# Performance work log

Hardware: AMD Instinct MI355X
Metric: run time of the kernel (lower is better)

## Reference

```python
import jax, jax.numpy as jnp
import numpy as np

D_MODEL = 1024
NHEAD = 16
HEAD_DIM = D_MODEL // NHEAD
WINDOW = 33  # mask keeps |i-j| > WINDOW//2 (True = attend, matching torch SDPA bool-mask semantics)


def setup_inputs() -> dict:
    key = jax.random.key(0)
    ks = jax.random.split(key, 9)
    s = 1.0 / np.sqrt(D_MODEL)
    x = jax.random.normal(ks[0], (2, 2048, D_MODEL), dtype=jnp.float32)
    Wq = jax.random.uniform(ks[1], (D_MODEL, D_MODEL), jnp.float32, -s, s)
    bq = jax.random.uniform(ks[2], (D_MODEL,), jnp.float32, -s, s)
    Wk = jax.random.uniform(ks[3], (D_MODEL, D_MODEL), jnp.float32, -s, s)
    bk = jax.random.uniform(ks[4], (D_MODEL,), jnp.float32, -s, s)
    Wv = jax.random.uniform(ks[5], (D_MODEL, D_MODEL), jnp.float32, -s, s)
    bv = jax.random.uniform(ks[6], (D_MODEL,), jnp.float32, -s, s)
    Wo = jax.random.uniform(ks[7], (D_MODEL, D_MODEL), jnp.float32, -s, s)
    bo = jax.random.uniform(ks[8], (D_MODEL,), jnp.float32, -s, s)
    return {"x": x, "Wq": Wq, "bq": bq, "Wk": Wk, "bk": bk,
            "Wv": Wv, "bv": bv, "Wo": Wo, "bo": bo}


def reference(x, Wq, bq, Wk, bk, Wv, bv, Wo, bo):
    B, T, C = x.shape
    H, D = NHEAD, HEAD_DIM
    # projections (torch Linear: y = x @ W.T + b)
    q = (x @ Wq.T + bq).reshape(B, T, H, D).transpose(0, 2, 1, 3)  # [B,H,T,D]
    k = (x @ Wk.T + bk).reshape(B, T, H, D).transpose(0, 2, 1, 3)
    v = (x @ Wv.T + bv).reshape(B, T, H, D).transpose(0, 2, 1, 3)
    idx = jnp.arange(T)
    rel = jnp.abs(idx[:, None] - idx[None, :])
    keep = rel > (WINDOW // 2)  # True = participate (torch SDPA bool-mask semantics)
    scale = 1.0 / jnp.sqrt(jnp.asarray(D, dtype=x.dtype))
    scores = jnp.einsum('bhqd,bhkd->bhqk', q, k) * scale
    scores = jnp.where(keep, scores, jnp.asarray(-jnp.inf, dtype=scores.dtype))
    attn = jax.nn.softmax(scores, axis=-1)
    out = jnp.einsum('bhqk,bhkd->bhqd', attn, v)  # [B,H,T,D]
    out = out.transpose(0, 2, 1, 3).reshape(B, T, C)
    return out @ Wo.T + bo
```

## Files before the change

kernel.cpp:

```cpp
#include <hip/hip_runtime.h>
#include <stdint.h>


typedef unsigned short u16;
typedef short bf16x8 __attribute__((ext_vector_type(8)));
typedef float f32x4 __attribute__((ext_vector_type(4)));

#define MFMA16 __builtin_amdgcn_mfma_f32_16x16x32_bf16

__device__ __forceinline__ u16 f2bf(float f) {
  union { float f; uint32_t u; } v; v.f = f;
  return (u16)((v.u + 0x7fffu + ((v.u >> 16) & 1u)) >> 16);
}

__device__ __forceinline__ uint32_t cvt_pk_bf16(float lo, float hi) {
  uint32_t d;
  asm("v_cvt_pk_bf16_f32 %0, %1, %2" : "=v"(d) : "v"(lo), "v"(hi));
  return d;
}

__global__ void f2b_kernel(const float* __restrict__ in, u16* __restrict__ out, int n4) {
  int i = blockIdx.x * blockDim.x + threadIdx.x;
  if (i < n4) {
    float4 v = reinterpret_cast<const float4*>(in)[i];
    ushort4 o;
    o.x = f2bf(v.x); o.y = f2bf(v.y); o.z = f2bf(v.z); o.w = f2bf(v.w);
    reinterpret_cast<ushort4*>(out)[i] = o;
  }
}

__global__ void f2b4_kernel(const float* __restrict__ a, const float* __restrict__ b,
                            const float* __restrict__ c, const float* __restrict__ d,
                            u16* __restrict__ oa, u16* __restrict__ ob,
                            u16* __restrict__ oc, u16* __restrict__ od, int n4) {
  int i = blockIdx.x * blockDim.x + threadIdx.x;
  if (i >= n4) return;
  int w = blockIdx.y;
  const float* src = (w == 0) ? a : (w == 1) ? b : (w == 2) ? c : d;
  u16* dst = (w == 0) ? oa : (w == 1) ? ob : (w == 2) ? oc : od;
  float4 v = reinterpret_cast<const float4*>(src)[i];
  ushort4 o;
  o.x = f2bf(v.x); o.y = f2bf(v.y); o.z = f2bf(v.z); o.w = f2bf(v.w);
  reinterpret_cast<ushort4*>(dst)[i] = o;
}

#define GEMM_LOAD(REGA, REGB, A_, B_, KOFF)                                                        \
  do {                                                                                             \
    REGA##0 = *reinterpret_cast<const uint4*>(A_ + (size_t)(gm_base +  0) * 1024 + (KOFF) + sslot * 8); \
    REGA##1 = *reinterpret_cast<const uint4*>(A_ + (size_t)(gm_base + 32) * 1024 + (KOFF) + sslot * 8); \
    REGA##2 = *reinterpret_cast<const uint4*>(A_ + (size_t)(gm_base + 64) * 1024 + (KOFF) + sslot * 8); \
    REGA##3 = *reinterpret_cast<const uint4*>(A_ + (size_t)(gm_base + 96) * 1024 + (KOFF) + sslot * 8); \
    REGB##0 = *reinterpret_cast<const uint4*>(B_ + (size_t)(gn_base +  0) * 1024 + (KOFF) + sslot * 8); \
    REGB##1 = *reinterpret_cast<const uint4*>(B_ + (size_t)(gn_base + 32) * 1024 + (KOFF) + sslot * 8); \
    REGB##2 = *reinterpret_cast<const uint4*>(B_ + (size_t)(gn_base + 64) * 1024 + (KOFF) + sslot * 8); \
    REGB##3 = *reinterpret_cast<const uint4*>(B_ + (size_t)(gn_base + 96) * 1024 + (KOFF) + sslot * 8); \
  } while (0)

#define GEMM_PUBLISH()                                                                             \
  do {                                                                                             \
    *reinterpret_cast<uint4*>((char*)As + (srow +  0) * 144 + sslot * 16) = ar0;                   \
    *reinterpret_cast<uint4*>((char*)As + (srow + 32) * 144 + sslot * 16) = ar1;                   \
    *reinterpret_cast<uint4*>((char*)As + (srow + 64) * 144 + sslot * 16) = ar2;                   \
    *reinterpret_cast<uint4*>((char*)As + (srow + 96) * 144 + sslot * 16) = ar3;                   \
    *reinterpret_cast<uint4*>((char*)Bs + (srow +  0) * 144 + sslot * 16) = br0;                   \
    *reinterpret_cast<uint4*>((char*)Bs + (srow + 32) * 144 + sslot * 16) = br1;                   \
    *reinterpret_cast<uint4*>((char*)Bs + (srow + 64) * 144 + sslot * 16) = br2;                   \
    *reinterpret_cast<uint4*>((char*)Bs + (srow + 96) * 144 + sslot * 16) = br3;                   \
  } while (0)

#define GEMM_CORE(A_, B_, bm0_, bn0_)                                                              \
  constexpr int KP = 72;                                                                           \
  __shared__ __align__(16) u16 As[128 * KP];                                                       \
  __shared__ __align__(16) u16 Bs[128 * KP];                                                       \
  const int t = threadIdx.x;                                                                       \
  const int lane = t & 63;                                                                         \
  const int wv = t >> 6;                                                                           \
  const int wm = (wv >> 1) * 64;                                                                   \
  const int wn = (wv & 1) * 64;                                                                    \
  const int lg = lane >> 4;                                                                        \
  const int lr = lane & 15;                                                                        \
  const int srow = t >> 3;                                                                         \
  const int sslot = t & 7;                                                                         \
  const int gm_base = bm0_ + srow;                                                                 \
  const int gn_base = bn0_ + srow;                                                                 \
  uint4 ar0, ar1, ar2, ar3, br0, br1, br2, br3;                                                    \
  f32x4 acc[4][4];                                                                                 \
  for (int i = 0; i < 4; ++i)                                                                      \
    for (int j = 0; j < 4; ++j) acc[i][j] = (f32x4)0.0f;                                           \
  GEMM_LOAD(ar, br, A_, B_, 0);                                                                    \
  for (int k0 = 0; k0 < 1024; k0 += 64) {                                                          \
    GEMM_PUBLISH();                                                                                \
    __syncthreads();                                                                               \
    if (k0 + 64 < 1024) GEMM_LOAD(ar, br, A_, B_, k0 + 64);                                        \
    for (int kk = 0; kk < 2; ++kk) {                                                               \
      bf16x8 af[4], bfr[4];                                                                        \
      for (int i = 0; i < 4; ++i)                                                                  \
        af[i] = *reinterpret_cast<const bf16x8*>(&As[(wm + i * 16 + lr) * KP + kk * 32 + lg * 8]); \
      for (int j = 0; j < 4; ++j)                                                                  \
        bfr[j] = *reinterpret_cast<const bf16x8*>(&Bs[(wn + j * 16 + lr) * KP + kk * 32 + lg * 8]);\
      for (int i = 0; i < 4; ++i)                                                                  \
        for (int j = 0; j < 4; ++j)                                                                \
          acc[i][j] = MFMA16(af[i], bfr[j], acc[i][j], 0, 0, 0);                                   \
    }                                                                                              \
    __syncthreads();                                                                               \
  }

__global__ __launch_bounds__(256) void gemm_qkv(
    const u16* __restrict__ A,
    const u16* __restrict__ Wqb, const u16* __restrict__ Wkb, const u16* __restrict__ Wvb,
    const float* __restrict__ bqp, const float* __restrict__ bkp, const float* __restrict__ bvp,
    u16* __restrict__ qo, u16* __restrict__ ko, u16* __restrict__ vo)
{
  const int bid = blockIdx.x + gridDim.x * blockIdx.y;
  const int sid = (bid & 7) * 96 + (bid >> 3);
  const int bm0 = (sid / 24) * 128;
  const int jy = sid % 24;
  const int sel = jy >> 3;
  const int bn0 = (jy & 7) * 128;

  const u16* Bw = (sel == 0) ? Wqb : (sel == 1) ? Wkb : Wvb;
  const float* bias = (sel == 0) ? bqp : (sel == 1) ? bkp : bvp;
  const float scale = (sel == 0) ? 0.125f * 1.44269504f : 1.0f;

  GEMM_CORE(A, Bw, bm0, bn0)

  for (int j = 0; j < 4; ++j) {
    int gn = bn0 + wn + j * 16 + lr;
    float bv = bias[gn];
    for (int i = 0; i < 4; ++i) {
      for (int r = 0; r < 4; ++r) {
        int gm = bm0 + wm + i * 16 + lg * 4 + r;
        float val = (acc[i][j][r] + bv) * scale;
        int b = gm >> 11, tt = gm & 2047;
        int h = gn >> 6,  d = gn & 63;
        u16 o = f2bf(val);
        if (sel == 0)
          qo[((size_t)(b * 16 + h) * 2048 + tt) * 64 + d] = o;
        else if (sel == 1)
          ko[((size_t)(b * 16 + h) * 2048 + tt) * 64 + d] = o;
        else
          vo[((size_t)(b * 16 + h) * 64 + d) * 2048 + tt] = o;
      }
    }
  }
}

__global__ __launch_bounds__(256) void gemm_out(
    const u16* __restrict__ A, const u16* __restrict__ Bw,
    const float* __restrict__ bias, float* __restrict__ outp)
{
  const int bm0 = blockIdx.x * 128;
  const int bn0 = blockIdx.y * 128;

  GEMM_CORE(A, Bw, bm0, bn0)

  for (int j = 0; j < 4; ++j) {
    int gn = bn0 + wn + j * 16 + lr;
    float bv = bias[gn];
    for (int i = 0; i < 4; ++i)
      for (int r = 0; r < 4; ++r) {
        int gm = bm0 + wm + i * 16 + lg * 4 + r;
        outp[(size_t)gm * 1024 + gn] = acc[i][j][r] + bv;
      }
  }
}

__global__ __launch_bounds__(256, 3) void attn_kernel(
    const u16* __restrict__ qb, const u16* __restrict__ kb,
    const u16* __restrict__ vtb, u16* __restrict__ ab)
{
  constexpr int KP = 72;
  __shared__ __align__(16) u16 Kb[2][64 * KP];
  __shared__ __align__(16) u16 Vb[2][64 * KP];
  __shared__ __align__(16) u16 Pl[4][16 * 64];

  const int bid = blockIdx.x + gridDim.x * blockIdx.y;
  const int sid = (bid & 7) * 128 + (bid >> 3);
  const int bx = sid & 31;
  const int bh = sid >> 5;

  const int t = threadIdx.x;
  const int lane = t & 63;
  const int wv = t >> 6;
  const int lg = lane >> 4, lr = lane & 15;
  const int q0 = bx * 64 + wv * 16;

  const u16* Qp = qb + (size_t)bh * 2048 * 64;
  const u16* Kp = kb + (size_t)bh * 2048 * 64;
  const u16* Vt = vtb + (size_t)bh * 64 * 2048;
  char* Pw = (char*)&Pl[wv][0];
  const int swz = (lr & 7) << 4;

  const int sl = lane & 7;
  const int r0 = wv * 16 + (lane >> 3);
  const int sdst0 = r0 * (KP * 2) + sl * 16;

  uint4 krA, krB, vrA, vrB;

#define ISSUE_LOADS(J0N)                                                                 \
  do {                                                                                   \
    krA = *reinterpret_cast<const uint4*>(Kp + (size_t)((J0N) + r0) * 64 + sl * 8);      \
    krB = *reinterpret_cast<const uint4*>(Kp + (size_t)((J0N) + r0 + 8) * 64 + sl * 8);  \
    vrA = *reinterpret_cast<const uint4*>(Vt + (size_t)r0 * 2048 + (J0N) + sl * 8);      \
    vrB = *reinterpret_cast<const uint4*>(Vt + (size_t)(r0 + 8) * 2048 + (J0N) + sl * 8);\
  } while (0)

#define WRITE_LDS(BUF)                                                                   \
  do {                                                                                   \
    *reinterpret_cast<uint4*>((char*)&Kb[BUF][0] + sdst0)                = krA;          \
    *reinterpret_cast<uint4*>((char*)&Kb[BUF][0] + sdst0 + 8 * KP * 2)   = krB;          \
    *reinterpret_cast<uint4*>((char*)&Vb[BUF][0] + sdst0)                = vrA;          \
    *reinterpret_cast<uint4*>((char*)&Vb[BUF][0] + sdst0 + 8 * KP * 2)   = vrB;          \
  } while (0)

  bf16x8 qf0 = *reinterpret_cast<const bf16x8*>(&Qp[(size_t)(q0 + lr) * 64 + lg * 8]);
  bf16x8 qf1 = *reinterpret_cast<const bf16x8*>(&Qp[(size_t)(q0 + lr) * 64 + 32 + lg * 8]);

  f32x4 o[4];
  for (int d = 0; d < 4; ++d) o[d] = (f32x4)0.0f;
  float m = -1e30f;
  float lsum = 0.0f;

  ISSUE_LOADS(0);
  WRITE_LDS(0);
  __syncthreads();
  int cur = 0;

  for (int tt = 0; tt < 32; ++tt) {
    if (tt < 31) ISSUE_LOADS((tt + 1) * 64);
    const int j0 = tt * 64;

    f32x4 s[4];
    for (int kc = 0; kc < 4; ++kc) {
      bf16x8 kf0 = *reinterpret_cast<const bf16x8*>(&Kb[cur][(kc * 16 + lr) * KP + lg * 8]);
      bf16x8 kf1 = *reinterpret_cast<const bf16x8*>(&Kb[cur][(kc * 16 + lr) * KP + 32 + lg * 8]);
      f32x4 z = (f32x4)0.0f;
      z = MFMA16(kf0, qf0, z, 0, 0, 0);
      z = MFMA16(kf1, qf1, z, 0, 0, 0);
      s[kc] = z;
    }
    if (j0 + 63 >= q0 - 16 && j0 <= q0 + 31) {
      for (int kc = 0; kc < 4; ++kc)
        for (int r = 0; r < 4; ++r) {
          int i = q0 + lr;
          int j = j0 + kc * 16 + lg * 4 + r;
          int dd = i - j; if (dd < 0) dd = -dd;
          if (dd <= 16) s[kc][r] = -1e38f;
        }
    }
    f32x4 t4 = __builtin_elementwise_max(__builtin_elementwise_max(s[0], s[1]),
                                         __builtin_elementwise_max(s[2], s[3]));
    float pm = fmaxf(fmaxf(t4[0], t4[1]), fmaxf(t4[2], t4[3]));
    pm = fmaxf(pm, __shfl_xor(pm, 16));
    pm = fmaxf(pm, __shfl_xor(pm, 32));
    if (__any((int)(pm > m + 11.54f))) {
      float mn = fmaxf(m, pm);
      float a = exp2f(m - mn);
      m = mn;
      lsum *= a;
      for (int d = 0; d < 4; ++d) o[d] *= a;
    }
    for (int kc = 0; kc < 4; ++kc) {
      float p0 = exp2f(s[kc][0] - m);
      float p1 = exp2f(s[kc][1] - m);
      float p2 = exp2f(s[kc][2] - m);
      float p3 = exp2f(s[kc][3] - m);
      lsum += (p0 + p1) + (p2 + p3);
      uint2 pk;
      pk.x = cvt_pk_bf16(p0, p1);
      pk.y = cvt_pk_bf16(p2, p3);
      *reinterpret_cast<uint2*>(Pw + ((lr * 128 + kc * 32 + lg * 8) ^ swz)) = pk;
    }
    asm volatile("s_waitcnt lgkmcnt(0)" ::: "memory");
    for (int kh = 0; kh < 2; ++kh) {
      bf16x8 pa = *reinterpret_cast<const bf16x8*>(
          Pw + ((lr * 128 + kh * 64 + lg * 16) ^ swz));
      for (int d = 0; d < 4; ++d) {
        bf16x8 vf = *reinterpret_cast<const bf16x8*>(
            &Vb[cur][(d * 16 + lr) * KP + kh * 32 + lg * 8]);
        o[d] = MFMA16(vf, pa, o[d], 0, 0, 0);
      }
    }
    if (tt < 31) WRITE_LDS(cur ^ 1);
    __syncthreads();
    cur ^= 1;
  }

  lsum += __shfl_xor(lsum, 16);
  lsum += __shfl_xor(lsum, 32);
  float inv = 1.0f / lsum;
  int b = bh >> 4, h = bh & 15;
  size_t rowoff = ((size_t)b * 2048 + q0 + lr) * 1024 + h * 64;
  for (int d = 0; d < 4; ++d) {
    uint2 pk;
    pk.x = cvt_pk_bf16(o[d][0] * inv, o[d][1] * inv);
    pk.y = cvt_pk_bf16(o[d][2] * inv, o[d][3] * inv);
    *reinterpret_cast<uint2*>(&ab[rowoff + d * 16 + lg * 4]) = pk;
  }
#undef ISSUE_LOADS
#undef WRITE_LDS
}

extern "C" void kernel_launch(void* const* d_in, const int* in_sizes, int n_in,
                              void* d_out, int out_size, void* d_ws, size_t ws_size,
                              hipStream_t stream) {
  const float* x  = (const float*)d_in[0];
  const float* Wq = (const float*)d_in[1];
  const float* bq = (const float*)d_in[2];
  const float* Wk = (const float*)d_in[3];
  const float* bk = (const float*)d_in[4];
  const float* Wv = (const float*)d_in[5];
  const float* bv = (const float*)d_in[6];
  const float* Wo = (const float*)d_in[7];
  const float* bo = (const float*)d_in[8];

  u16* ws  = (u16*)d_ws;
  u16* xb  = ws;
  u16* wqb = ws + 4194304;
  u16* wkb = ws + 5242880;
  u16* wvb = ws + 6291456;
  u16* wob = ws + 7340032;
  u16* qbf = ws + 8388608;
  u16* kbf = ws + 12582912;
  u16* vbf = ws + 16777216;
  u16* ab  = xb;

  f2b_kernel<<<4096, 256, 0, stream>>>(x, xb, 1048576);
  f2b4_kernel<<<dim3(1024, 4), 256, 0, stream>>>(Wq, Wk, Wv, Wo, wqb, wkb, wvb, wob, 262144);

  gemm_qkv<<<dim3(32, 24), 256, 0, stream>>>(xb, wqb, wkb, wvb, bq, bk, bv, qbf, kbf, vbf);

  attn_kernel<<<dim3(32, 32), 256, 0, stream>>>(qbf, kbf, vbf, ab);

  gemm_out<<<dim3(32, 8), 256, 0, stream>>>(ab, wob, bo, (float*)d_out);
}
```

Before: 161.3 us.

## Switch attention to 32x32 MFMA tiles with 128-query blocks

The attention kernel now uses 32x32x16 bf16 MFMA. Each wave handles 32 query rows instead of 16 and each block handles 128 queries, so the grid is halved. This doubles the reuse of every K/V tile loaded into LDS and cuts per-tile LDS traffic and global reloads. It also replaces exp2f with the raw v_exp_f32 instruction and drops the occupancy hint from launch bounds, at the cost of more registers per wave and fewer blocks to spread across CUs.

```diff
diff --git a/kernel.cpp b/kernel.cpp
--- a/kernel.cpp
+++ b/kernel.cpp
@@ -5,8 +5,10 @@
 typedef unsigned short u16;
 typedef short bf16x8 __attribute__((ext_vector_type(8)));
 typedef float f32x4 __attribute__((ext_vector_type(4)));
+typedef float f32x16 __attribute__((ext_vector_type(16)));
 
 #define MFMA16 __builtin_amdgcn_mfma_f32_16x16x32_bf16
+#define MFMA32 __builtin_amdgcn_mfma_f32_32x32x16_bf16
 
 __device__ __forceinline__ u16 f2bf(float f) {
   union { float f; uint32_t u; } v; v.f = f;
@@ -17,6 +19,12 @@
   uint32_t d;
   asm("v_cvt_pk_bf16_f32 %0, %1, %2" : "=v"(d) : "v"(lo), "v"(hi));
   return d;
+}
+
+__device__ __forceinline__ float hexp2(float x) {
+  float r;
+  asm("v_exp_f32 %0, %1" : "=v"(r) : "v"(x));
+  return r;
 }
 
 __global__ void f2b_kernel(const float* __restrict__ in, u16* __restrict__ out, int n4) {
@@ -165,31 +173,31 @@
   }
 }
 
-__global__ __launch_bounds__(256, 3) void attn_kernel(
+__global__ __launch_bounds__(256) void attn_kernel(
     const u16* __restrict__ qb, const u16* __restrict__ kb,
     const u16* __restrict__ vtb, u16* __restrict__ ab)
 {
   constexpr int KP = 72;
   __shared__ __align__(16) u16 Kb[2][64 * KP];
   __shared__ __align__(16) u16 Vb[2][64 * KP];
-  __shared__ __align__(16) u16 Pl[4][16 * 64];
+  __shared__ __align__(16) u16 Pl[4][32 * KP];
 
   const int bid = blockIdx.x + gridDim.x * blockIdx.y;
-  const int sid = (bid & 7) * 128 + (bid >> 3);
-  const int bx = sid & 31;
-  const int bh = sid >> 5;
+  const int sid = (bid & 7) * 64 + (bid >> 3);
+  const int bx = sid & 15;
+  const int bh = sid >> 4;
 
   const int t = threadIdx.x;
   const int lane = t & 63;
   const int wv = t >> 6;
-  const int lg = lane >> 4, lr = lane & 15;
-  const int q0 = bx * 64 + wv * 16;
+  const int ql = lane & 31;
+  const int hi = lane >> 5;
+  const int q0 = bx * 128 + wv * 32;
 
   const u16* Qp = qb + (size_t)bh * 2048 * 64;
   const u16* Kp = kb + (size_t)bh * 2048 * 64;
   const u16* Vt = vtb + (size_t)bh * 64 * 2048;
   char* Pw = (char*)&Pl[wv][0];
-  const int swz = (lr & 7) << 4;
 
   const int sl = lane & 7;
   const int r0 = wv * 16 + (lane >> 3);
@@ -213,11 +221,12 @@
     *reinterpret_cast<uint4*>((char*)&Vb[BUF][0] + sdst0 + 8 * KP * 2)   = vrB;          \
   } while (0)
 
-  bf16x8 qf0 = *reinterpret_cast<const bf16x8*>(&Qp[(size_t)(q0 + lr) * 64 + lg * 8]);
-  bf16x8 qf1 = *reinterpret_cast<const bf16x8*>(&Qp[(size_t)(q0 + lr) * 64 + 32 + lg * 8]);
-
-  f32x4 o[4];
-  for (int d = 0; d < 4; ++d) o[d] = (f32x4)0.0f;
+  bf16x8 qf0 = *reinterpret_cast<const bf16x8*>(&Qp[(size_t)(q0 + ql) * 64 +  0 + hi * 8]);
+  bf16x8 qf1 = *reinterpret_cast<const bf16x8*>(&Qp[(size_t)(q0 + ql) * 64 + 16 + hi * 8]);
+  bf16x8 qf2 = *reinterpret_cast<const bf16x8*>(&Qp[(size_t)(q0 + ql) * 64 + 32 + hi * 8]);
+  bf16x8 qf3 = *reinterpret_cast<const bf16x8*>(&Qp[(size_t)(q0 + ql) * 64 + 48 + hi * 8]);
+
+  f32x16 o0 = (f32x16)0.0f, o1 = (f32x16)0.0f;
   float m = -1e30f;
   float lsum = 0.0f;
 
@@ -230,72 +239,87 @@
     if (tt < 31) ISSUE_LOADS((tt + 1) * 64);
     const int j0 = tt * 64;
 
-    f32x4 s[4];
-    for (int kc = 0; kc < 4; ++kc) {
-      bf16x8 kf0 = *reinterpret_cast<const bf16x8*>(&Kb[cur][(kc * 16 + lr) * KP + lg * 8]);
-      bf16x8 kf1 = *reinterpret_cast<const bf16x8*>(&Kb[cur][(kc * 16 + lr) * KP + 32 + lg * 8]);
-      f32x4 z = (f32x4)0.0f;
-      z = MFMA16(kf0, qf0, z, 0, 0, 0);
-      z = MFMA16(kf1, qf1, z, 0, 0, 0);
-      s[kc] = z;
-    }
-    if (j0 + 63 >= q0 - 16 && j0 <= q0 + 31) {
-      for (int kc = 0; kc < 4; ++kc)
-        for (int r = 0; r < 4; ++r) {
-          int i = q0 + lr;
-          int j = j0 + kc * 16 + lg * 4 + r;
-          int dd = i - j; if (dd < 0) dd = -dd;
-          if (dd <= 16) s[kc][r] = -1e38f;
-        }
-    }
-    f32x4 t4 = __builtin_elementwise_max(__builtin_elementwise_max(s[0], s[1]),
-                                         __builtin_elementwise_max(s[2], s[3]));
-    float pm = fmaxf(fmaxf(t4[0], t4[1]), fmaxf(t4[2], t4[3]));
-    pm = fmaxf(pm, __shfl_xor(pm, 16));
+    f32x16 s0 = (f32x16)0.0f, s1 = (f32x16)0.0f;
+    {
+      bf16x8 kf;
+#define QK_STEP(KB, KC, QF, SACC)                                                        \
+      kf = *reinterpret_cast<const bf16x8*>(&Kb[cur][((KB) * 32 + ql) * KP + (KC) * 16 + hi * 8]); \
+      SACC = MFMA32(kf, QF, SACC, 0, 0, 0);
+      QK_STEP(0, 0, qf0, s0) QK_STEP(0, 1, qf1, s0) QK_STEP(0, 2, qf2, s0) QK_STEP(0, 3, qf3, s0)
+      QK_STEP(1, 0, qf0, s1) QK_STEP(1, 1, qf1, s1) QK_STEP(1, 2, qf2, s1) QK_STEP(1, 3, qf3, s1)
+#undef QK_STEP
+    }
+    if (j0 + 63 >= q0 - 16 && j0 <= q0 + 47) {
+      const int i = q0 + ql;
+#pragma unroll
+      for (int reg = 0; reg < 16; ++reg) {
+        int kl = (reg & 3) + 8 * (reg >> 2) + 4 * hi;
+        int d0 = i - (j0 + kl);      if (d0 < 0) d0 = -d0;
+        int d1 = i - (j0 + 32 + kl); if (d1 < 0) d1 = -d1;
+        if (d0 <= 16) s0[reg] = -1e38f;
+        if (d1 <= 16) s1[reg] = -1e38f;
+      }
+    }
+    f32x16 tm = __builtin_elementwise_max(s0, s1);
+    float pm = fmaxf(fmaxf(fmaxf(fmaxf(tm[0], tm[1]), fmaxf(tm[2], tm[3])),
+                           fmaxf(fmaxf(tm[4], tm[5]), fmaxf(tm[6], tm[7]))),
+                     fmaxf(fmaxf(fmaxf(tm[8], tm[9]), fmaxf(tm[10], tm[11])),
+                           fmaxf(fmaxf(tm[12], tm[13]), fmaxf(tm[14], tm[15]))));
     pm = fmaxf(pm, __shfl_xor(pm, 32));
     if (__any((int)(pm > m + 11.54f))) {
       float mn = fmaxf(m, pm);
-      float a = exp2f(m - mn);
+      float a = hexp2(m - mn);
       m = mn;
       lsum *= a;
-      for (int d = 0; d < 4; ++d) o[d] *= a;
-    }
-    for (int kc = 0; kc < 4; ++kc) {
-      float p0 = exp2f(s[kc][0] - m);
-      float p1 = exp2f(s[kc][1] - m);
-      float p2 = exp2f(s[kc][2] - m);
-      float p3 = exp2f(s[kc][3] - m);
-      lsum += (p0 + p1) + (p2 + p3);
-      uint2 pk;
-      pk.x = cvt_pk_bf16(p0, p1);
-      pk.y = cvt_pk_bf16(p2, p3);
-      *reinterpret_cast<uint2*>(Pw + ((lr * 128 + kc * 32 + lg * 8) ^ swz)) = pk;
+      o0 *= a;
+      o1 *= a;
+    }
+    {
+      float psum = 0.0f;
+      char* prow = Pw + ql * (KP * 2);
+#pragma unroll
+      for (int qd = 0; qd < 4; ++qd) {
+        float a0 = hexp2(s0[4 * qd + 0] - m), a1 = hexp2(s0[4 * qd + 1] - m);
+        float a2 = hexp2(s0[4 * qd + 2] - m), a3 = hexp2(s0[4 * qd + 3] - m);
+        float b0 = hexp2(s1[4 * qd + 0] - m), b1 = hexp2(s1[4 * qd + 1] - m);
+        float b2 = hexp2(s1[4 * qd + 2] - m), b3 = hexp2(s1[4 * qd + 3] - m);
+        psum += ((a0 + a1) + (a2 + a3)) + ((b0 + b1) + (b2 + b3));
+        uint2 pkA, pkB;
+        pkA.x = cvt_pk_bf16(a0, a1); pkA.y = cvt_pk_bf16(a2, a3);
+        pkB.x = cvt_pk_bf16(b0, b1); pkB.y = cvt_pk_bf16(b2, b3);
+        *reinterpret_cast<uint2*>(prow + (8 * qd + 4 * hi) * 2)      = pkA;
+        *reinterpret_cast<uint2*>(prow + (32 + 8 * qd + 4 * hi) * 2) = pkB;
+      }
+      lsum += psum;
     }
     asm volatile("s_waitcnt lgkmcnt(0)" ::: "memory");
-    for (int kh = 0; kh < 2; ++kh) {
-      bf16x8 pa = *reinterpret_cast<const bf16x8*>(
-          Pw + ((lr * 128 + kh * 64 + lg * 16) ^ swz));
-      for (int d = 0; d < 4; ++d) {
-        bf16x8 vf = *reinterpret_cast<const bf16x8*>(
-            &Vb[cur][(d * 16 + lr) * KP + kh * 32 + lg * 8]);
-        o[d] = MFMA16(vf, pa, o[d], 0, 0, 0);
-      }
+#pragma unroll
+    for (int s = 0; s < 4; ++s) {
+      bf16x8 pf = *reinterpret_cast<const bf16x8*>(Pw + ql * (KP * 2) + (s * 16 + hi * 8) * 2);
+      bf16x8 vf0 = *reinterpret_cast<const bf16x8*>(&Vb[cur][(ql) * KP + s * 16 + hi * 8]);
+      bf16x8 vf1 = *reinterpret_cast<const bf16x8*>(&Vb[cur][(32 + ql) * KP + s * 16 + hi * 8]);
+      o0 = MFMA32(vf0, pf, o0, 0, 0, 0);
+      o1 = MFMA32(vf1, pf, o1, 0, 0, 0);
     }
     if (tt < 31) WRITE_LDS(cur ^ 1);
     __syncthreads();
     cur ^= 1;
   }
 
-  lsum += __shfl_xor(lsum, 16);
   lsum += __shfl_xor(lsum, 32);
   float inv = 1.0f / lsum;
   int b = bh >> 4, h = bh & 15;
-  size_t rowoff = ((size_t)b * 2048 + q0 + lr) * 1024 + h * 64;
-  for (int d = 0; d < 4; ++d) {
-    uint2 pk;
-    pk.x = cvt_pk_bf16(o[d][0] * inv, o[d][1] * inv);
-    pk.y = cvt_pk_bf16(o[d][2] * inv, o[d][3] * inv);
-    *reinterpret_cast<uint2*>(&ab[rowoff + d * 16 + lg * 4]) = pk;
+  size_t rowoff = ((size_t)b * 2048 + q0 + ql) * 1024 + h * 64;
+#pragma unroll
+  for (int qd = 0; qd < 4; ++qd) {
+    int d0 = 8 * qd + 4 * hi;
+    uint2 pk0, pk1;
+    pk0.x = cvt_pk_bf16(o0[4 * qd + 0] * inv, o0[4 * qd + 1] * inv);
+    pk0.y = cvt_pk_bf16(o0[4 * qd + 2] * inv, o0[4 * qd + 3] * inv);
+    pk1.x = cvt_pk_bf16(o1[4 * qd + 0] * inv, o1[4 * qd + 1] * inv);
+    pk1.y = cvt_pk_bf16(o1[4 * qd + 2] * inv, o1[4 * qd + 3] * inv);
+    *reinterpret_cast<uint2*>(&ab[rowoff + d0])      = pk0;
+    *reinterpret_cast<uint2*>(&ab[rowoff + 32 + d0]) = pk1;
   }
 #undef ISSUE_LOADS
 #undef WRITE_LDS
@@ -330,7 +354,7 @@
 
   gemm_qkv<<<dim3(32, 24), 256, 0, stream>>>(xb, wqb, wkb, wvb, bq, bk, bv, qbf, kbf, vbf);
 
-  attn_kernel<<<dim3(32, 32), 256, 0, stream>>>(qbf, kbf, vbf, ab);
+  attn_kernel<<<dim3(16, 32), 256, 0, stream>>>(qbf, kbf, vbf, ab);
 
   gemm_out<<<dim3(32, 8), 256, 0, stream>>>(ab, wob, bo, (float*)d_out);
 }
```

After: 144.6 us. -10.4%, faster.
